# Performance work log

Measured on AMD Instinct MI355X. Metric: run time of the kernel, lower is better.

The kernel has to match this reference:

```python
import jax, jax.numpy as jnp
import numpy as np

SURROGATE_SCALE = 10.0  # SuperSpike-style surrogate slope

@jax.custom_vjp
def spike_fn(v):
    # Heaviside forward (standard SNN spike function)
    return (v > 0).astype(v.dtype)

def _spike_fwd(v):
    return spike_fn(v), v

def _spike_bwd(v, g):
    surrogate = 1.0 / (SURROGATE_SCALE * jnp.abs(v) + 1.0) ** 2
    return (g * surrogate,)

spike_fn.defvjp(_spike_fwd, _spike_bwd)

def setup_inputs() -> dict:
    key = jax.random.key(0)
    B, C, T = 128, 512, 1024
    x = jax.random.normal(key, (B, C, T), dtype=jnp.float32)
    beta = jnp.asarray(0.65, dtype=jnp.float32)   # scalar leak (non-trainable default)
    Vth = jnp.ones((C,), dtype=jnp.float32)        # threshold per channel
    return {"x": x, "beta": beta, "Vth": Vth}

def reference(x, beta, Vth):
    # x: (B, C, T)  -- time_position=2, negative_mempot=True, flatten_output=False
    B, C, T = x.shape
    xs = jnp.moveaxis(x, 2, 0)  # (T, B, C): scan over time

    def step(carry, inp):
        mem, spk = carry
        rst = spk * Vth                 # einsum('ab,b->ab', spk, Vth)
        mem = mem * beta + inp - rst    # negative_mempot branch
        spk = spike_fn(mem - Vth)
        return (mem, spk), spk

    init = (jnp.zeros((B, C), x.dtype), jnp.zeros((B, C), x.dtype))
    _, spk_rec = jax.lax.scan(step, init, xs)   # (T, B, C)
    return jnp.moveaxis(spk_rec, 0, 2)          # (B, C, T)
```

## Files before the change

### kernel.cpp

```cpp
#include <hip/hip_runtime.h>


#define LIF_BC 65536
#define LIF_T  1024
#define TT     128
#define NT     (LIF_T / TT)
#define ROWS   64
#define GPT    (TT / 4)

using fvec4 = __attribute__((ext_vector_type(4))) float;

__global__ __launch_bounds__(64) void lif_fwd(
    const float* __restrict__ x,
    const float* __restrict__ beta_p,
    const float* __restrict__ vth_p,
    float* __restrict__ out)
{
    __shared__ float lds[ROWS * TT];

    const int lane = threadIdx.x;
    const int r0   = blockIdx.x * ROWS;

    const float beta = beta_p[0];
    const float vth  = vth_p[(r0 + lane) & 511];

    const int l_row2 = lane >> 5;
    const int l_t    = lane & 31;

    fvec4 pf[GPT];

    auto issue_loads = [&](int tile) {
#pragma unroll
        for (int j = 0; j < GPT; ++j) {
            const int row = 2 * j + l_row2;
            pf[j] = __builtin_nontemporal_load(
                (const fvec4*)&x[(size_t)(r0 + row) * LIF_T
                                 + (size_t)tile * TT + l_t * 4]);
        }
    };

    auto write_lds = [&]() {
#pragma unroll
        for (int j = 0; j < GPT; ++j) {
            const int row  = 2 * j + l_row2;
            const int slot = (l_t & 16) | ((l_t & 15) ^ (row & 15));
            *(fvec4*)&lds[row * TT + slot * 4] = pf[j];
        }
    };

    float mem = 0.0f, spk = 0.0f;

    auto compute = [&]() {
        const int rbase = lane * TT;
        const int sw    = lane & 15;
#pragma unroll
        for (int g = 0; g < GPT; ++g) {
            const int slot = (g & 16) | ((g & 15) ^ sw);
            fvec4 v = *(fvec4*)&lds[rbase + slot * 4];
#pragma unroll
            for (int e = 0; e < 4; ++e) {
                float rst = __fmul_rn(spk, vth);
                mem = __fsub_rn(__fadd_rn(__fmul_rn(mem, beta), v[e]), rst);
                spk = (__fsub_rn(mem, vth) > 0.0f) ? 1.0f : 0.0f;
                v[e] = spk;
            }
            *(fvec4*)&lds[rbase + slot * 4] = v;
        }
    };

    auto store_tile = [&](int tile) {
#pragma unroll
        for (int j = 0; j < GPT; ++j) {
            const int row  = 2 * j + l_row2;
            const int slot = (l_t & 16) | ((l_t & 15) ^ (row & 15));
            fvec4 s = *(const fvec4*)&lds[row * TT + slot * 4];
            __builtin_nontemporal_store(
                s, (fvec4*)&out[(size_t)(r0 + row) * LIF_T
                                + (size_t)tile * TT + l_t * 4]);
        }
    };

    issue_loads(0);
    write_lds();
    issue_loads(1);

    for (int k = 0; k < NT; ++k) {
        compute();
        store_tile(k);
        if (k + 1 < NT) write_lds();
        if (k + 2 < NT) issue_loads(k + 2);
    }
}

extern "C" void kernel_launch(void* const* d_in, const int* in_sizes, int n_in,
                              void* d_out, int out_size, void* d_ws, size_t ws_size,
                              hipStream_t stream) {
    const float* x    = (const float*)d_in[0];
    const float* beta = (const float*)d_in[1];
    const float* vth  = (const float*)d_in[2];
    float* out = (float*)d_out;

    dim3 grid(LIF_BC / ROWS);
    lif_fwd<<<grid, 64, 0, stream>>>(x, beta, vth, out);
}
```

Baseline: 474.8 us.

## Shrink rows per block to 16 with 256-step chunks to raise wave count

Each block now processes 16 rows in 256-timestep chunks instead of 64 rows in 128-step tiles. This quadruples the number of blocks, so more waves run per CU to hide the latency of the serial recurrence and the memory traffic. Only 16 of 64 lanes execute the scan, so three quarters of the SIMD lanes sit idle during compute. Global loads now cover a full 1KB contiguous row segment per instruction, and the LDS swizzle changes to a simple XOR by row.

Result: no change. 466.6 us (-1.7%).

```diff
diff --git a/kernel.cpp b/kernel.cpp
--- a/kernel.cpp
+++ b/kernel.cpp
@@ -3,10 +3,10 @@
 
 #define LIF_BC 65536
 #define LIF_T  1024
-#define TT     128
-#define NT     (LIF_T / TT)
-#define ROWS   64
-#define GPT    (TT / 4)
+#define CHUNK  256
+#define NP     (LIF_T / CHUNK)
+#define ROWS   16
+#define JPT    ROWS
 
 using fvec4 = __attribute__((ext_vector_type(4))) float;
 
@@ -16,7 +16,7 @@
     const float* __restrict__ vth_p,
     float* __restrict__ out)
 {
-    __shared__ float lds[ROWS * TT];
+    __shared__ float lds[ROWS * CHUNK];
 
     const int lane = threadIdx.x;
     const int r0   = blockIdx.x * ROWS;
@@ -24,59 +24,55 @@
     const float beta = beta_p[0];
     const float vth  = vth_p[(r0 + lane) & 511];
 
-    const int l_row2 = lane >> 5;
-    const int l_t    = lane & 31;
+    fvec4 pf[JPT];
 
-    fvec4 pf[GPT];
-
-    auto issue_loads = [&](int tile) {
+    auto issue_loads = [&](int ph) {
 #pragma unroll
-        for (int j = 0; j < GPT; ++j) {
-            const int row = 2 * j + l_row2;
+        for (int j = 0; j < JPT; ++j) {
             pf[j] = __builtin_nontemporal_load(
-                (const fvec4*)&x[(size_t)(r0 + row) * LIF_T
-                                 + (size_t)tile * TT + l_t * 4]);
+                (const fvec4*)&x[(size_t)(r0 + j) * LIF_T
+                                 + (size_t)ph * CHUNK + lane * 4]);
         }
     };
 
     auto write_lds = [&]() {
 #pragma unroll
-        for (int j = 0; j < GPT; ++j) {
-            const int row  = 2 * j + l_row2;
-            const int slot = (l_t & 16) | ((l_t & 15) ^ (row & 15));
-            *(fvec4*)&lds[row * TT + slot * 4] = pf[j];
+        for (int j = 0; j < JPT; ++j) {
+            const int slot = lane ^ j;
+            *(fvec4*)&lds[j * CHUNK + slot * 4] = pf[j];
         }
     };
 
     float mem = 0.0f, spk = 0.0f;
 
     auto compute = [&]() {
-        const int rbase = lane * TT;
-        const int sw    = lane & 15;
+        if (lane < ROWS) {
+            const int rbase = lane * CHUNK;
+            const int sw    = lane;
 #pragma unroll
-        for (int g = 0; g < GPT; ++g) {
-            const int slot = (g & 16) | ((g & 15) ^ sw);
-            fvec4 v = *(fvec4*)&lds[rbase + slot * 4];
+            for (int g = 0; g < CHUNK / 4; ++g) {
+                const int slot = g ^ sw;
+                fvec4 v = *(fvec4*)&lds[rbase + slot * 4];
 #pragma unroll
-            for (int e = 0; e < 4; ++e) {
-                float rst = __fmul_rn(spk, vth);
-                mem = __fsub_rn(__fadd_rn(__fmul_rn(mem, beta), v[e]), rst);
-                spk = (__fsub_rn(mem, vth) > 0.0f) ? 1.0f : 0.0f;
-                v[e] = spk;
+                for (int e = 0; e < 4; ++e) {
+                    float rst = __fmul_rn(spk, vth);
+                    mem = __fsub_rn(__fadd_rn(__fmul_rn(mem, beta), v[e]), rst);
+                    spk = (__fsub_rn(mem, vth) > 0.0f) ? 1.0f : 0.0f;
+                    v[e] = spk;
+                }
+                *(fvec4*)&lds[rbase + slot * 4] = v;
             }
-            *(fvec4*)&lds[rbase + slot * 4] = v;
         }
     };
 
-    auto store_tile = [&](int tile) {
+    auto store_tile = [&](int ph) {
 #pragma unroll
-        for (int j = 0; j < GPT; ++j) {
-            const int row  = 2 * j + l_row2;
-            const int slot = (l_t & 16) | ((l_t & 15) ^ (row & 15));
-            fvec4 s = *(const fvec4*)&lds[row * TT + slot * 4];
+        for (int j = 0; j < JPT; ++j) {
+            const int slot = lane ^ j;
+            fvec4 s = *(const fvec4*)&lds[j * CHUNK + slot * 4];
             __builtin_nontemporal_store(
-                s, (fvec4*)&out[(size_t)(r0 + row) * LIF_T
-                                + (size_t)tile * TT + l_t * 4]);
+                s, (fvec4*)&out[(size_t)(r0 + j) * LIF_T
+                                + (size_t)ph * CHUNK + lane * 4]);
         }
     };
 
@@ -84,11 +80,11 @@
     write_lds();
     issue_loads(1);
 
-    for (int k = 0; k < NT; ++k) {
+    for (int k = 0; k < NP; ++k) {
         compute();
         store_tile(k);
-        if (k + 1 < NT) write_lds();
-        if (k + 2 < NT) issue_loads(k + 2);
+        if (k + 1 < NP) write_lds();
+        if (k + 2 < NP) issue_loads(k + 2);
     }
 }
 
```
